# Performance work log

Hardware: AMD Instinct MI355X
Metric: run time of the kernel (lower is better)

## Reference

```python
import jax, jax.numpy as jnp
import numpy as np

B, T, N, D, H = 8, 24, 512, 128, 8
HD = D // H
HID = int(D * 2.0)
SCALES = (1.0, 0.01)


def _l2norm(a):
    # F.normalize(dim=-1), eps=1e-12
    n = jnp.sqrt(jnp.sum(a * a, axis=-1, keepdims=True))
    return a / jnp.maximum(n, 1e-12)


def _layernorm(a, g, b):
    mu = a.mean(-1, keepdims=True)
    var = ((a - mu) ** 2).mean(-1, keepdims=True)
    return (a - mu) / jnp.sqrt(var + 1e-5) * g + b


def _fast_attention_layer(z, qkv_w, out_w, out_b):
    # z: [B,T,N,D]; qkv_w: [D,3D]; out_w: [2D,D]; out_b: [D]
    b, t, n, d = z.shape
    q, k, v = jnp.split(z @ qkv_w, 3, axis=-1)          # each [B,T,N,D]
    q = q.reshape(b, t, n, H, HD)
    k = k.reshape(b, t, n, H, HD)
    v = v.reshape(b, t, n, H, HD)
    qn = _l2norm(q)
    kn = _l2norm(k)
    # spatial linear attention (tokens = nodes, axis 2)
    kvs = jnp.einsum('btnhm,btnhd->bthmd', kn, v)
    num = jnp.einsum('btnhm,bthmd->btnhd', qn, kvs) + n * v
    den = jnp.einsum('btnhm,bthm->btnh', qn, kn.sum(axis=2))[..., None] + n
    out_s = (num / den).reshape(b, t, n, d)
    # temporal linear attention (tokens = time steps, axis 1)
    kvt = jnp.einsum('btnhm,btnhd->bnhmd', kn, v)
    numt = jnp.einsum('btnhm,bnhmd->btnhd', qn, kvt) + t * v
    dent = jnp.einsum('btnhm,bnhm->btnh', qn, kn.sum(axis=1))[..., None] + t
    out_t = (numt / dent).reshape(b, t, n, d)
    return jnp.concatenate([out_s, out_t], axis=-1) @ out_w + out_b


def setup_inputs() -> dict:
    key = jax.random.key(0)
    ks = jax.random.split(key, 20)
    s = 0.02
    inp = {
        'x': jax.random.normal(ks[0], (B, T, N, D), jnp.float32),
        'graph': jax.random.uniform(ks[1], (T, N, N), jnp.float32) / N,
        'qkv_w0': jax.random.normal(ks[2], (D, 3 * D), jnp.float32) * s,
        'out_w0': jax.random.normal(ks[3], (2 * D, D), jnp.float32) * s,
        'out_b0': jnp.zeros((D,), jnp.float32),
        'pw_w0': jax.random.normal(ks[4], (D, D), jnp.float32) * s,
        'pw_b0': jax.random.normal(ks[5], (D,), jnp.float32) * s,
        'qkv_w1': jax.random.normal(ks[6], (D, 3 * D), jnp.float32) * s,
        'out_w1': jax.random.normal(ks[7], (2 * D, D), jnp.float32) * s,
        'out_b1': jnp.zeros((D,), jnp.float32),
        'pw_w1': jax.random.normal(ks[8], (D, D), jnp.float32) * s,
        'pw_b1': jax.random.normal(ks[9], (D,), jnp.float32) * s,
        'fc1_w': jax.random.normal(ks[10], (D, HID), jnp.float32) * s,
        'fc1_b': jnp.zeros((HID,), jnp.float32),
        'fc2_w': jax.random.normal(ks[11], (HID, D), jnp.float32) * s,
        'fc2_b': jnp.zeros((D,), jnp.float32),
        'ln1_g': jnp.ones((D,), jnp.float32),
        'ln1_b': jnp.zeros((D,), jnp.float32),
        'ln2_g': jnp.ones((D,), jnp.float32),
        'ln2_b': jnp.zeros((D,), jnp.float32),
    }
    return inp


def reference(x, graph, qkv_w0, out_w0, out_b0, pw_w0, pw_b0,
              qkv_w1, out_w1, out_b1, pw_w1, pw_b1,
              fc1_w, fc1_b, fc2_w, fc2_b, ln1_g, ln1_b, ln2_g, ln2_b):
    # GraphPropagate (Ks=order=2): x_loc = [x, graph @ x]; dropout in eval mode
    x1 = jnp.einsum('tni,btid->btnd', graph, x)
    x_loc = (x, x1)
    layer_params = ((qkv_w0, out_w0, out_b0, pw_w0, pw_b0),
                    (qkv_w1, out_w1, out_b1, pw_w1, pw_b1))
    c = x
    x_glo = x
    for k in range(2):
        qkv_w, out_w, out_b, pw_w, pw_b = layer_params[k]
        att = _fast_attention_layer(x_loc[k], qkv_w, out_w, out_b)
        pw = c @ pw_w + pw_b
        x_glo = x_glo + att * pw * SCALES[k]
        c = att
    h = _layernorm(x + x_glo, ln1_g, ln1_b)
    mlp = jax.nn.relu(h @ fc1_w + fc1_b) @ fc2_w + fc2_b
    return _layernorm(h + mlp, ln2_g, ln2_b)
```

## Files before the change

### kernel.cpp

```cpp
#include <hip/hip_runtime.h>
#include <cstddef>

#define Bb 8
#define Tt 24
#define Nn 512
#define Dd 128
#define Hh 8

typedef unsigned short u16;
using short8 = __attribute__((ext_vector_type(8))) short;
using f32x4  = __attribute__((ext_vector_type(4))) float;

__device__ __forceinline__ float b2f(u16 u) {
  union { unsigned u; float f; } w; w.u = ((unsigned)u) << 16; return w.f;
}
__device__ __forceinline__ u16 f2b(float f) {
  union { float f; unsigned u; } w; w.f = f;
  unsigned r = w.u + 0x7FFFu + ((w.u >> 16) & 1u);
  return (u16)(r >> 16);
}

__device__ __forceinline__ void mm_phase(const u16* __restrict__ A,
                                         const u16* __restrict__ BT,
                                         int K, int m0,
                                         u16* sA, u16* sB, f32x4 acc[4][4])
{
  const int tid = threadIdx.x;
  const int l = tid & 63, wid = tid >> 6;
  const int wm = (wid >> 1) << 6, wn = (wid & 1) << 6;
  int a_off[4], b_off[4];
#pragma unroll
  for (int i = 0; i < 4; ++i) {
    int ra = wm + i * 16 + (l & 15);
    a_off[i] = ((ra << 6) + ((l >> 4) << 4)) ^ ((ra & 7) << 4);
    int rb = wn + i * 16 + (l & 15);
    b_off[i] = ((rb << 6) + ((l >> 4) << 4)) ^ ((rb & 7) << 4);
  }
  const int r0 = tid >> 2, s0 = tid & 3;
  const int r1 = r0 + 64;
  const int w0 = ((r0 << 6) + (s0 << 4)) ^ ((r0 & 7) << 4);
  const int w1 = ((r1 << 6) + (s0 << 4)) ^ ((r1 & 7) << 4);
  const size_t aR0 = (size_t)(m0 + r0) * K, aR1 = (size_t)(m0 + r1) * K;
  const size_t bR0 = (size_t)r0 * K, bR1 = (size_t)r1 * K;
  const int ks = s0 * 8;
  for (int k0 = 0; k0 < K; k0 += 32) {
    short8 a0 = *(const short8*)(A + aR0 + k0 + ks);
    short8 a1 = *(const short8*)(A + aR1 + k0 + ks);
    short8 b0 = *(const short8*)(BT + bR0 + k0 + ks);
    short8 b1 = *(const short8*)(BT + bR1 + k0 + ks);
    __syncthreads();
    *(short8*)((char*)sA + w0) = a0;
    *(short8*)((char*)sA + w1) = a1;
    *(short8*)((char*)sB + w0) = b0;
    *(short8*)((char*)sB + w1) = b1;
    __syncthreads();
    short8 af[4], bf_[4];
#pragma unroll
    for (int i = 0; i < 4; ++i) {
      af[i]  = *(const short8*)((const char*)sA + a_off[i]);
      bf_[i] = *(const short8*)((const char*)sB + b_off[i]);
    }
#pragma unroll
    for (int mi = 0; mi < 4; ++mi)
#pragma unroll
      for (int ni = 0; ni < 4; ++ni)
        acc[mi][ni] = __builtin_amdgcn_mfma_f32_16x16x32_bf16(
            af[mi], bf_[ni], acc[mi][ni], 0, 0, 0);
  }
}

template <int OUTBF16, int RELU>
__device__ __forceinline__ void gemm_mfma_body(
    const u16* __restrict__ A, const u16* __restrict__ BT,
    const float* __restrict__ bias, void* __restrict__ Cv,
    int N, int K, int m0, int n0)
{
  __shared__ u16 sA[4096];
  __shared__ u16 sB[4096];
  f32x4 acc[4][4] = {};
  mm_phase(A, BT + (size_t)n0 * K, K, m0, sA, sB, acc);
  const int l = threadIdx.x & 63, wid = threadIdx.x >> 6;
  const int wm = (wid >> 1) << 6, wn = (wid & 1) << 6;
  const int cr = (l >> 4) << 2, cc = l & 15;
#pragma unroll
  for (int mi = 0; mi < 4; ++mi) {
    int rowb = m0 + wm + mi * 16 + cr;
#pragma unroll
    for (int ni = 0; ni < 4; ++ni) {
      int col = n0 + wn + ni * 16 + cc;
      float bb = bias ? bias[col] : 0.f;
#pragma unroll
      for (int r = 0; r < 4; ++r) {
        float v = acc[mi][ni][r] + bb;
        if (RELU) v = fmaxf(v, 0.f);
        size_t idx = (size_t)(rowb + r) * N + col;
        if (OUTBF16) ((u16*)Cv)[idx] = f2b(v);
        else         ((float*)Cv)[idx] = v;
      }
    }
  }
}

template <int OUTBF16, int RELU>
__global__ __launch_bounds__(256) void gemm_mfma_k(
    const u16* __restrict__ A, const u16* __restrict__ BT,
    const float* __restrict__ bias, void* __restrict__ C, int N, int K)
{
  gemm_mfma_body<OUTBF16, RELU>(A, BT, bias, C, N, K,
                                blockIdx.y * 128, blockIdx.x * 128);
}

__global__ __launch_bounds__(256) void gemm_mfma_graph(
    const u16* __restrict__ g, const u16* __restrict__ xT, u16* __restrict__ x1)
{
  const int bt = blockIdx.z, t = bt % Tt;
  gemm_mfma_body<1, 0>(g + (size_t)t * Nn * Nn, xT + (size_t)bt * Dd * Nn,
                       nullptr, x1 + (size_t)bt * Nn * Dd,
                       Dd, Nn, blockIdx.y * 128, 0);
}

__global__ __launch_bounds__(256) void gemm_og0(
    const u16* __restrict__ cat, const u16* __restrict__ outT, const float* __restrict__ ob,
    const u16* __restrict__ xb,  const u16* __restrict__ pwT,  const float* __restrict__ pb,
    u16* __restrict__ gp0, u16* __restrict__ att0)
{
  __shared__ u16 sA[4096], sB[4096];
  const int m0 = blockIdx.x * 128;
  f32x4 accP[4][4] = {};
  mm_phase(xb, pwT, 128, m0, sA, sB, accP);
  f32x4 accO[4][4] = {};
  mm_phase(cat, outT, 256, m0, sA, sB, accO);
  const int l = threadIdx.x & 63, wid = threadIdx.x >> 6;
  const int wm = (wid >> 1) << 6, wn = (wid & 1) << 6;
  const int cr = (l >> 4) << 2, cc = l & 15;
#pragma unroll
  for (int mi = 0; mi < 4; ++mi) {
    int rowb = m0 + wm + mi * 16 + cr;
#pragma unroll
    for (int ni = 0; ni < 4; ++ni) {
      int col = wn + ni * 16 + cc;
      float obv = ob[col], pbv = pb[col];
#pragma unroll
      for (int r = 0; r < 4; ++r) {
        size_t idx = (size_t)(rowb + r) * 128 + col;
        float attv = accO[mi][ni][r] + obv;
        float pwv  = accP[mi][ni][r] + pbv;
        att0[idx] = f2b(attv);
        gp0[idx] = f2b(attv * pwv);
      }
    }
  }
}

__global__ __launch_bounds__(256) void gemm_og1(
    const u16* __restrict__ cat, const u16* __restrict__ outT, const float* __restrict__ ob,
    const u16* __restrict__ att0, const u16* __restrict__ pwT, const float* __restrict__ pb,
    const u16* __restrict__ gp0, const float* __restrict__ x,
    const float* __restrict__ g, const float* __restrict__ be,
    u16* __restrict__ h16)
{
  __shared__ __align__(16) u16 smem[128 * 136];
  __shared__ float sg[128], sbt[128];
  u16* sA = smem;
  u16* sB = smem + 4096;
  if (threadIdx.x < 128) { sg[threadIdx.x] = g[threadIdx.x]; sbt[threadIdx.x] = be[threadIdx.x]; }
  const int m0 = blockIdx.x * 128;
  f32x4 accP[4][4] = {};
  mm_phase(att0, pwT, 128, m0, sA, sB, accP);
  f32x4 accO[4][4] = {};
  mm_phase(cat, outT, 256, m0, sA, sB, accO);
  const int l = threadIdx.x & 63, wid = threadIdx.x >> 6;
  const int wm = (wid >> 1) << 6, wn = (wid & 1) << 6;
  const int cr = (l >> 4) << 2, cc = l & 15;
  __syncthreads();
#pragma unroll
  for (int mi = 0; mi < 4; ++mi) {
    int lrow = wm + mi * 16 + cr;
#pragma unroll
    for (int ni = 0; ni < 4; ++ni) {
      int col = wn + ni * 16 + cc;
      float obv = ob[col], pbv = pb[col];
#pragma unroll
      for (int r = 0; r < 4; ++r) {
        size_t idx = (size_t)(m0 + lrow + r) * 128 + col;
        float attv = accO[mi][ni][r] + obv;
        float pwv  = accP[mi][ni][r] + pbv;
        float hpre = 2.f * x[idx] + b2f(gp0[idx]) + attv * pwv * 0.01f;
        smem[(lrow + r) * 136 + col] = f2b(hpre);
      }
    }
  }
  __syncthreads();
  const int row = threadIdx.x >> 1, half = threadIdx.x & 1;
  const u16* rp = smem + row * 136 + half * 64;
  float s = 0.f, ss = 0.f;
#pragma unroll
  for (int j8 = 0; j8 < 8; ++j8) {
    short8 v = *(const short8*)(rp + j8 * 8);
#pragma unroll
    for (int j = 0; j < 8; ++j) { float f = b2f((u16)v[j]); s += f; ss += f * f; }
  }
  s += __shfl_xor(s, 1);
  ss += __shfl_xor(ss, 1);
  float mu = s * (1.f / 128.f);
  float rstd = rsqrtf(ss * (1.f / 128.f) - mu * mu + 1e-5f);
  size_t gbase = (size_t)(m0 + row) * 128 + half * 64;
#pragma unroll
  for (int j8 = 0; j8 < 8; ++j8) {
    short8 v = *(const short8*)(rp + j8 * 8);
    short8 o;
#pragma unroll
    for (int j = 0; j < 8; ++j) {
      int col = half * 64 + j8 * 8 + j;
      o[j] = (short)f2b((b2f((u16)v[j]) - mu) * rstd * sg[col] + sbt[col]);
    }
    *(short8*)(h16 + gbase + j8 * 8) = o;
  }
}

__global__ __launch_bounds__(256) void gemm_fc2ln(
    const u16* __restrict__ hid, const u16* __restrict__ fc2T, const float* __restrict__ fb,
    const u16* __restrict__ h16, const float* __restrict__ g, const float* __restrict__ be,
    float* __restrict__ out)
{
  __shared__ __align__(16) u16 smem[128 * 136];
  __shared__ float sg[128], sbt[128];
  u16* sA = smem;
  u16* sB = smem + 4096;
  if (threadIdx.x < 128) { sg[threadIdx.x] = g[threadIdx.x]; sbt[threadIdx.x] = be[threadIdx.x]; }
  const int m0 = blockIdx.x * 128;
  f32x4 accO[4][4] = {};
  mm_phase(hid, fc2T, 256, m0, sA, sB, accO);
  const int l = threadIdx.x & 63, wid = threadIdx.x >> 6;
  const int wm = (wid >> 1) << 6, wn = (wid & 1) << 6;
  const int cr = (l >> 4) << 2, cc = l & 15;
  __syncthreads();
#pragma unroll
  for (int mi = 0; mi < 4; ++mi) {
    int lrow = wm + mi * 16 + cr;
#pragma unroll
    for (int ni = 0; ni < 4; ++ni) {
      int col = wn + ni * 16 + cc;
      float fbv = fb[col];
#pragma unroll
      for (int r = 0; r < 4; ++r) {
        size_t idx = (size_t)(m0 + lrow + r) * 128 + col;
        float hpre = b2f(h16[idx]) + accO[mi][ni][r] + fbv;
        smem[(lrow + r) * 136 + col] = f2b(hpre);
      }
    }
  }
  __syncthreads();
  const int row = threadIdx.x >> 1, half = threadIdx.x & 1;
  const u16* rp = smem + row * 136 + half * 64;
  float s = 0.f, ss = 0.f;
#pragma unroll
  for (int j8 = 0; j8 < 8; ++j8) {
    short8 v = *(const short8*)(rp + j8 * 8);
#pragma unroll
    for (int j = 0; j < 8; ++j) { float f = b2f((u16)v[j]); s += f; ss += f * f; }
  }
  s += __shfl_xor(s, 1);
  ss += __shfl_xor(ss, 1);
  float mu = s * (1.f / 128.f);
  float rstd = rsqrtf(ss * (1.f / 128.f) - mu * mu + 1e-5f);
  size_t gbase = (size_t)(m0 + row) * 128 + half * 64;
#pragma unroll
  for (int j8 = 0; j8 < 8; ++j8) {
    short8 v = *(const short8*)(rp + j8 * 8);
    float4 o0, o1;
#pragma unroll
    for (int j = 0; j < 8; ++j) {
      int col = half * 64 + j8 * 8 + j;
      float y = (b2f((u16)v[j]) - mu) * rstd * sg[col] + sbt[col];
      if (j < 4) ((float*)&o0)[j] = y; else ((float*)&o1)[j - 4] = y;
    }
    *(float4*)(out + gbase + j8 * 8) = o0;
    *(float4*)(out + gbase + j8 * 8 + 4) = o1;
  }
}

__global__ __launch_bounds__(256) void qknorm(const u16* __restrict__ qkv,
                                              float* __restrict__ inv, size_t nidx)
{
  size_t idx = (size_t)blockIdx.x * 256 + threadIdx.x;
  if (idx >= nidx) return;
  size_t row = idx >> 4;
  int g = (int)(idx & 15);
  const u16* p = qkv + row * 384 + g * 16;
  short8 a = *(const short8*)p;
  short8 b = *(const short8*)(p + 8);
  float ss = 0.f;
#pragma unroll
  for (int j = 0; j < 8; ++j) {
    float f0 = b2f((u16)a[j]), f1 = b2f((u16)b[j]);
    ss += f0 * f0 + f1 * f1;
  }
  inv[idx] = 1.f / fmaxf(sqrtf(ss), 1e-12f);
}

__global__ __launch_bounds__(256) void cvt_f32_bf16(const float* __restrict__ src,
                                                    u16* __restrict__ dst, size_t n8)
{
  size_t i = (size_t)blockIdx.x * 256 + threadIdx.x;
  if (i >= n8) return;
  const float4* s = (const float4*)src;
  float4 u = s[i * 2], v = s[i * 2 + 1];
  short8 o;
  o[0] = (short)f2b(u.x); o[1] = (short)f2b(u.y);
  o[2] = (short)f2b(u.z); o[3] = (short)f2b(u.w);
  o[4] = (short)f2b(v.x); o[5] = (short)f2b(v.y);
  o[6] = (short)f2b(v.z); o[7] = (short)f2b(v.w);
  *(short8*)(dst + i * 8) = o;
}

__global__ __launch_bounds__(256) void transpose_cvt(const float* __restrict__ src,
                                                     u16* __restrict__ dst,
                                                     int R, int C)
{
  __shared__ u16 tile[64][65];
  const int tid = threadIdx.x;
  src += (size_t)blockIdx.z * R * C;
  dst += (size_t)blockIdx.z * R * C;
  const int c0 = blockIdx.x * 64, r0 = blockIdx.y * 64;
  const int tx = tid & 63, ty = tid >> 6;
#pragma unroll
  for (int i = 0; i < 64; i += 4)
    tile[ty + i][tx] = f2b(src[(size_t)(r0 + ty + i) * C + c0 + tx]);
  __syncthreads();
#pragma unroll
  for (int i = 0; i < 64; i += 4)
    dst[(size_t)(c0 + ty + i) * R + r0 + tx] = tile[tx][ty + i];
}

__global__ __launch_bounds__(256) void cvt_transpose_x(const float* __restrict__ src,
                                                       u16* __restrict__ xb,
                                                       u16* __restrict__ xT)
{
  __shared__ u16 tile[64][65];
  const int tid = threadIdx.x;
  const size_t zo = (size_t)blockIdx.z * Nn * Dd;
  src += zo; xb += zo; xT += zo;
  const int c0 = blockIdx.x * 64, r0 = blockIdx.y * 64;
  const int tx = tid & 63, ty = tid >> 6;
#pragma unroll
  for (int i = 0; i < 64; i += 4) {
    u16 b = f2b(src[(size_t)(r0 + ty + i) * Dd + c0 + tx]);
    tile[ty + i][tx] = b;
    xb[(size_t)(r0 + ty + i) * Dd + c0 + tx] = b;
  }
  __syncthreads();
#pragma unroll
  for (int i = 0; i < 64; i += 4)
    xT[(size_t)(c0 + ty + i) * Nn + r0 + tx] = tile[tx][ty + i];
}

__global__ __launch_bounds__(256) void spatial_stats(const u16* __restrict__ qkv,
                                                     const float* __restrict__ qkn,
                                                     float* __restrict__ kvs2,
                                                     float* __restrict__ ksum)
{
  __shared__ u16 sKT[16 * 512];
  __shared__ u16 sVT[16 * 512];
  __shared__ float red[4][16][16];
  __shared__ float red2[4][16];
  const int bt = blockIdx.x, h = blockIdx.y;
  const int tid = threadIdx.x;

  u16 kr[2][16], vr[2][16];
#pragma unroll
  for (int r = 0; r < 2; ++r) {
    int n = tid * 2 + r;
    size_t rowg = (size_t)bt * 512 + n;
    size_t base = rowg * 384;
    float inv = qkn[rowg * 16 + 8 + h];
    short8 k0 = *(const short8*)(qkv + base + 128 + h * 16);
    short8 k1 = *(const short8*)(qkv + base + 136 + h * 16);
    short8 v0 = *(const short8*)(qkv + base + 256 + h * 16);
    short8 v1 = *(const short8*)(qkv + base + 264 + h * 16);
#pragma unroll
    for (int j = 0; j < 8; ++j) {
      kr[r][j]     = f2b(b2f((u16)k0[j]) * inv);
      kr[r][j + 8] = f2b(b2f((u16)k1[j]) * inv);
      vr[r][j] = (u16)v0[j]; vr[r][j + 8] = (u16)v1[j];
    }
  }
#pragma unroll
  for (int m = 0; m < 16; ++m) {
    unsigned pk = (unsigned)kr[0][m] | ((unsigned)kr[1][m] << 16);
    unsigned pv = (unsigned)vr[0][m] | ((unsigned)vr[1][m] << 16);
    int wa = ((m << 10) + (tid << 2)) ^ ((m & 7) << 4);
    *(unsigned*)((char*)sKT + wa) = pk;
    *(unsigned*)((char*)sVT + wa) = pv;
  }
  __syncthreads();

  const int l = tid & 63, w = tid >> 6;
  const int fr = l & 15, tq = l >> 4;
  short8 ones;
#pragma unroll
  for (int j = 0; j < 8; ++j) ones[j] = (short)0x3F80;
  f32x4 acc = {}, acs = {};
#pragma unroll
  for (int kk = 0; kk < 4; ++kk) {
    int noff = w * 128 + kk * 32 + tq * 8;
    int ra = ((fr << 10) + (noff << 1)) ^ ((fr & 7) << 4);
    short8 afr = *(const short8*)((const char*)sKT + ra);
    short8 bfr = *(const short8*)((const char*)sVT + ra);
    acc = __builtin_amdgcn_mfma_f32_16x16x32_bf16(afr, bfr, acc, 0, 0, 0);
    acs = __builtin_amdgcn_mfma_f32_16x16x32_bf16(afr, ones, acs, 0, 0, 0);
  }
#pragma unroll
  for (int r = 0; r < 4; ++r) red[w][tq * 4 + r][fr] = acc[r];
  if (fr == 0) {
#pragma unroll
    for (int r = 0; r < 4; ++r) red2[w][tq * 4 + r] = acs[r];
  }
  __syncthreads();
  const size_t o = (size_t)bt * 8 + h;
  {
    int m = tid >> 4, d = tid & 15;
    float s = red[0][m][d] + red[1][m][d] + red[2][m][d] + red[3][m][d];
    kvs2[o * 256 + d * 16 + m] = s;
  }
  if (tid < 16) {
    float s = red2[0][tid] + red2[1][tid] + red2[2][tid] + red2[3][tid];
    ksum[o * 16 + tid] = s;
  }
}

__global__ __launch_bounds__(256) void temporal_stats(const u16* __restrict__ qkv,
                                                      const float* __restrict__ qkn,
                                                      float* __restrict__ kvt,
                                                      float* __restrict__ kst)
{
  __shared__ u16 sKT[128 * 32];
  __shared__ u16 sVT[128 * 32];
  const int nn = blockIdx.x, b = blockIdx.y;
  const int tid = threadIdx.x;
  if (tid < 128) {
    short8 z = {};
    int wa = ((tid << 6) + 48) ^ ((tid & 3) << 4);
    *(short8*)((char*)sKT + wa) = z;
    *(short8*)((char*)sVT + wa) = z;
  }
  for (int idx = tid; idx < 384; idx += 256) {
    int t = idx >> 4, c8 = idx & 15;
    size_t rowg = ((size_t)(b * 24 + t) * 512) + nn;
    float inv = qkn[rowg * 16 + 8 + (c8 >> 1)];
    short8 kv = *(const short8*)(qkv + rowg * 384 + 128 + c8 * 8);
    short8 vv = *(const short8*)(qkv + rowg * 384 + 256 + c8 * 8);
#pragma unroll
    for (int j = 0; j < 8; ++j) {
      int c = c8 * 8 + j;
      int wa = ((c << 6) + (t << 1)) ^ ((c & 3) << 4);
      *(u16*)((char*)sKT + wa) = f2b(b2f((u16)kv[j]) * inv);
      *(u16*)((char*)sVT + wa) = (u16)vv[j];
    }
  }
  __syncthreads();
  const int l = tid & 63, w = tid >> 6;
  const int fr = l & 15, tq = l >> 4;
  const size_t nb = (size_t)b * 512 + nn;
  short8 ones;
#pragma unroll
  for (int j = 0; j < 8; ++j) ones[j] = (short)0x3F80;
#pragma unroll
  for (int hi = 0; hi < 2; ++hi) {
    int h = w * 2 + hi;
    int c = h * 16 + fr;
    int ra = ((c << 6) + (tq << 4)) ^ ((c & 3) << 4);
    short8 afr = *(const short8*)((const char*)sKT + ra);
    short8 bfr = *(const short8*)((const char*)sVT + ra);
    f32x4 z = {};
    f32x4 acc = __builtin_amdgcn_mfma_f32_16x16x32_bf16(afr, bfr, z, 0, 0, 0);
    f32x4 acs = __builtin_amdgcn_mfma_f32_16x16x32_bf16(afr, ones, z, 0, 0, 0);
#pragma unroll
    for (int r = 0; r < 4; ++r)
      kvt[nb * 2048 + (size_t)(tq * 4 + r) * 128 + h * 16 + fr] = acc[r];
    if (fr == 0) {
#pragma unroll
      for (int r = 0; r < 4; ++r)
        kst[(nb * 8 + h) * 16 + tq * 4 + r] = acs[r];
    }
  }
}

__global__ __launch_bounds__(256) void attn_apply(const u16* __restrict__ qkv,
                                                  const float* __restrict__ qkn,
                                                  const float* __restrict__ kvs2,
                                                  const float* __restrict__ kss,
                                                  const float* __restrict__ kvt,
                                                  const float* __restrict__ kst,
                                                  u16* __restrict__ out_cat)
{
  __shared__ float s_kvt[2][2048];
  const int nn0 = blockIdx.x * 2, b = blockIdx.y;
  const int t0 = blockIdx.z * 8;
  const int tid = threadIdx.x;
  const int sub = tid >> 7, cl = tid & 127;
  const int nn = nn0 + sub;
  const size_t nb = (size_t)b * 512 + nn;
  for (int i = cl; i < 2048; i += 128) s_kvt[sub][i] = kvt[nb * 2048 + i];
  __syncthreads();
  const int hh = cl >> 4, d = cl & 15;
  const float kst_d = kst[(nb * 8 + hh) * 16 + d];
  for (int t = t0; t < t0 + 8; ++t) {
    const size_t row = ((size_t)(b * 24 + t) * 512) + nn;
    const u16* qp = qkv + row * 384 + hh * 16;
    short8 q0 = *(const short8*)qp;
    short8 q1 = *(const short8*)(qp + 8);
    const float inv = qkn[row * 16 + hh];
    float qf[16];
#pragma unroll
    for (int j = 0; j < 8; ++j) {
      qf[j] = b2f((u16)q0[j]);
      qf[j + 8] = b2f((u16)q1[j]);
    }
    const size_t sbase = ((size_t)(b * 24 + t) * 8 + hh) * 256 + d * 16;
    const float4* M4 = (const float4*)(kvs2 + sbase);
    float4 m0 = M4[0], m1 = M4[1], m2 = M4[2], m3 = M4[3];
    float accs = qf[0] * m0.x + qf[1] * m0.y + qf[2] * m0.z + qf[3] * m0.w;
    accs = fmaf(qf[4], m1.x, fmaf(qf[5], m1.y, fmaf(qf[6], m1.z, fmaf(qf[7], m1.w, accs))));
    accs = fmaf(qf[8], m2.x, fmaf(qf[9], m2.y, fmaf(qf[10], m2.z, fmaf(qf[11], m2.w, accs))));
    accs = fmaf(qf[12], m3.x, fmaf(qf[13], m3.y, fmaf(qf[14], m3.z, fmaf(qf[15], m3.w, accs))));
    float dps = qf[d] * kss[((size_t)(b * 24 + t) * 8 + hh) * 16 + d];
    dps += __shfl_xor(dps, 1);
    dps += __shfl_xor(dps, 2);
    dps += __shfl_xor(dps, 4);
    dps += __shfl_xor(dps, 8);
    float acct = 0.f;
#pragma unroll
    for (int mI = 0; mI < 16; ++mI)
      acct = fmaf(qf[mI], s_kvt[sub][mI * 128 + cl], acct);
    float dpt = qf[d] * kst_d;
    dpt += __shfl_xor(dpt, 1);
    dpt += __shfl_xor(dpt, 2);
    dpt += __shfl_xor(dpt, 4);
    dpt += __shfl_xor(dpt, 8);
    float vv = b2f(qkv[row * 384 + 256 + cl]);
    out_cat[row * 256 + cl]       = f2b((accs * inv + 512.f * vv) / (dps * inv + 512.f));
    out_cat[row * 256 + 128 + cl] = f2b((acct * inv + 24.f * vv) / (dpt * inv + 24.f));
  }
}

extern "C" void kernel_launch(void* const* d_in, const int* in_sizes, int n_in,
                              void* d_out, int out_size, void* d_ws, size_t ws_size,
                              hipStream_t stream)
{
  const float* x      = (const float*)d_in[0];
  const float* graph  = (const float*)d_in[1];
  const float* qkv_w0 = (const float*)d_in[2];
  const float* out_w0 = (const float*)d_in[3];
  const float* out_b0 = (const float*)d_in[4];
  const float* pw_w0  = (const float*)d_in[5];
  const float* pw_b0  = (const float*)d_in[6];
  const float* qkv_w1 = (const float*)d_in[7];
  const float* out_w1 = (const float*)d_in[8];
  const float* out_b1 = (const float*)d_in[9];
  const float* pw_w1  = (const float*)d_in[10];
  const float* pw_b1  = (const float*)d_in[11];
  const float* fc1_w  = (const float*)d_in[12];
  const float* fc1_b  = (const float*)d_in[13];
  const float* fc2_w  = (const float*)d_in[14];
  const float* fc2_b  = (const float*)d_in[15];
  const float* ln1_g  = (const float*)d_in[16];
  const float* ln1_b  = (const float*)d_in[17];
  const float* ln2_g  = (const float*)d_in[18];
  const float* ln2_b  = (const float*)d_in[19];
  float* out = (float*)d_out;

  auto al = [](size_t v) { return (v + 255) & ~(size_t)255; };
  const size_t Rb = 12288;
  const size_t fixed = al((size_t)Tt * Nn * Nn * 2) + 2 * al((size_t)384 * 128 * 2)
                     + 2 * al((size_t)128 * 256 * 2) + 2 * al((size_t)128 * 128 * 2)
                     + al((size_t)256 * 128 * 2) + al((size_t)128 * 256 * 2);
  const size_t perb = al(Rb * 768) + al(Rb * 512) + 4 * al(Rb * 256) + al(Rb * 512)
                    + al(Rb * 64)
                    + al((size_t)Tt * 8 * 256 * 4) + al((size_t)Tt * 8 * 16 * 4)
                    + al((size_t)Nn * 8 * 256 * 4) + al((size_t)Nn * 8 * 16 * 4);
  int CB = 8;
  while (CB > 1 && fixed + (size_t)CB * perb > ws_size) CB >>= 1;
  const size_t Mc = (size_t)CB * Rb;

  char* cur = (char*)d_ws;
  auto alloc = [&](size_t bytes) { char* p = cur; cur += (bytes + 255) & ~(size_t)255; return p; };
  u16* g_b16 = (u16*)alloc((size_t)Tt * Nn * Nn * 2);
  u16* qkvT0 = (u16*)alloc((size_t)384 * 128 * 2);
  u16* qkvT1 = (u16*)alloc((size_t)384 * 128 * 2);
  u16* outT0 = (u16*)alloc((size_t)128 * 256 * 2);
  u16* outT1 = (u16*)alloc((size_t)128 * 256 * 2);
  u16* pwT0  = (u16*)alloc((size_t)128 * 128 * 2);
  u16* pwT1  = (u16*)alloc((size_t)128 * 128 * 2);
  u16* fc1T  = (u16*)alloc((size_t)256 * 128 * 2);
  u16* fc2T  = (u16*)alloc((size_t)128 * 256 * 2);
  u16* qkvb  = (u16*)alloc(Mc * 768);
  u16* catb  = (u16*)alloc(Mc * 512);
  u16* x1b   = (u16*)alloc(Mc * 256);
  u16* att0  = (u16*)alloc(Mc * 256);
  u16* xb    = (u16*)alloc(Mc * 256);
  u16* xT    = (u16*)alloc(Mc * 256);
  u16* gp0   = (u16*)alloc(Mc * 512);
  float* qkn = (float*)alloc(Mc * 64);
  float* kvs = (float*)alloc((size_t)CB * Tt * 8 * 256 * 4);
  float* kss = (float*)alloc((size_t)CB * Tt * 8 * 16 * 4);
  float* kvt = (float*)alloc((size_t)CB * Nn * 8 * 256 * 4);
  float* kst = (float*)alloc((size_t)CB * Nn * 8 * 16 * 4);

  dim3 blk(256);
  cvt_f32_bf16<<<dim3((Tt * Nn * Nn / 8 + 255) / 256), blk, 0, stream>>>(
      graph, g_b16, (size_t)Tt * Nn * Nn / 8);
  transpose_cvt<<<dim3(6, 2, 1), blk, 0, stream>>>(qkv_w0, qkvT0, 128, 384);
  transpose_cvt<<<dim3(6, 2, 1), blk, 0, stream>>>(qkv_w1, qkvT1, 128, 384);
  transpose_cvt<<<dim3(2, 4, 1), blk, 0, stream>>>(out_w0, outT0, 256, 128);
  transpose_cvt<<<dim3(2, 4, 1), blk, 0, stream>>>(out_w1, outT1, 256, 128);
  transpose_cvt<<<dim3(2, 2, 1), blk, 0, stream>>>(pw_w0, pwT0, 128, 128);
  transpose_cvt<<<dim3(2, 2, 1), blk, 0, stream>>>(pw_w1, pwT1, 128, 128);
  transpose_cvt<<<dim3(4, 2, 1), blk, 0, stream>>>(fc1_w, fc1T, 128, 256);
  transpose_cvt<<<dim3(2, 4, 1), blk, 0, stream>>>(fc2_w, fc2T, 256, 128);

  const int MB = (int)(Mc / 128);
  const int nchunk = Bb / CB;
  for (int c = 0; c < nchunk; ++c) {
    const size_t off = (size_t)c * Mc * 128;
    const float* xc = x + off;
    float* outc = out + off;

    cvt_transpose_x<<<dim3(2, 8, CB * Tt), blk, 0, stream>>>(xc, xb, xT);
    gemm_mfma_graph<<<dim3(1, 4, CB * Tt), blk, 0, stream>>>(g_b16, xT, x1b);

    gemm_mfma_k<1, 0><<<dim3(3, MB), blk, 0, stream>>>(xb, qkvT0, nullptr, qkvb, 384, 128);
    qknorm<<<dim3((unsigned)(Mc / 16)), blk, 0, stream>>>(qkvb, qkn, Mc * 16);
    spatial_stats<<<dim3(CB * Tt, Hh), blk, 0, stream>>>(qkvb, qkn, kvs, kss);
    temporal_stats<<<dim3(Nn, CB), blk, 0, stream>>>(qkvb, qkn, kvt, kst);
    attn_apply<<<dim3(Nn / 2, CB, 3), blk, 0, stream>>>(qkvb, qkn, kvs, kss, kvt, kst, catb);
    gemm_og0<<<dim3(MB), blk, 0, stream>>>(catb, outT0, out_b0, xb, pwT0, pw_b0,
                                           gp0, att0);

    gemm_mfma_k<1, 0><<<dim3(3, MB), blk, 0, stream>>>(x1b, qkvT1, nullptr, qkvb, 384, 128);
    qknorm<<<dim3((unsigned)(Mc / 16)), blk, 0, stream>>>(qkvb, qkn, Mc * 16);
    spatial_stats<<<dim3(CB * Tt, Hh), blk, 0, stream>>>(qkvb, qkn, kvs, kss);
    temporal_stats<<<dim3(Nn, CB), blk, 0, stream>>>(qkvb, qkn, kvt, kst);
    attn_apply<<<dim3(Nn / 2, CB, 3), blk, 0, stream>>>(qkvb, qkn, kvs, kss, kvt, kst, catb);
    u16* h16 = qkvb;
    gemm_og1<<<dim3(MB), blk, 0, stream>>>(catb, outT1, out_b1, att0, pwT1, pw_b1,
                                           gp0, xc, ln1_g, ln1_b, h16);

    gemm_mfma_k<1, 1><<<dim3(2, MB), blk, 0, stream>>>(h16, fc1T, fc1_b, catb, 256, 128);
    gemm_fc2ln<<<dim3(MB), blk, 0, stream>>>(catb, fc2T, fc2_b, h16, ln2_g, ln2_b, outc);
  }

  (void)in_sizes; (void)n_in; (void)out_size;
}
```

Measured before the change: 658.0 us.

## Load GEMM tiles directly into LDS and streamline attention denominators

The GEMM main loop now uses global_load_lds to move A and B tiles straight from global memory into shared memory. This drops the register round trip and the XOR swizzle, so the LDS layout becomes plain row-major. In attn_apply, the spatial and temporal denominators are computed as full per-thread dot products from vectorized loads instead of butterfly shuffle reductions. Divisions are replaced with hardware reciprocals. Risks: the unswizzled LDS layout may cause bank conflicts on the fragment reads, the loads are no longer issued ahead of the barrier, and rcpf is less precise than a true divide.

```diff
diff --git a/kernel.cpp b/kernel.cpp
--- a/kernel.cpp
+++ b/kernel.cpp
@@ -20,6 +20,12 @@
   return (u16)(r >> 16);
 }
 
+__device__ __forceinline__ void gld16(const u16* g, u16* s) {
+  __builtin_amdgcn_global_load_lds(
+      (const __attribute__((address_space(1))) unsigned int*)g,
+      (__attribute__((address_space(3))) unsigned int*)s, 16, 0, 0);
+}
+
 __device__ __forceinline__ void mm_phase(const u16* __restrict__ A,
                                          const u16* __restrict__ BT,
                                          int K, int m0,
@@ -31,28 +37,23 @@
   int a_off[4], b_off[4];
 #pragma unroll
   for (int i = 0; i < 4; ++i) {
-    int ra = wm + i * 16 + (l & 15);
-    a_off[i] = ((ra << 6) + ((l >> 4) << 4)) ^ ((ra & 7) << 4);
-    int rb = wn + i * 16 + (l & 15);
-    b_off[i] = ((rb << 6) + ((l >> 4) << 4)) ^ ((rb & 7) << 4);
-  }
-  const int r0 = tid >> 2, s0 = tid & 3;
-  const int r1 = r0 + 64;
-  const int w0 = ((r0 << 6) + (s0 << 4)) ^ ((r0 & 7) << 4);
-  const int w1 = ((r1 << 6) + (s0 << 4)) ^ ((r1 & 7) << 4);
-  const size_t aR0 = (size_t)(m0 + r0) * K, aR1 = (size_t)(m0 + r1) * K;
-  const size_t bR0 = (size_t)r0 * K, bR1 = (size_t)r1 * K;
-  const int ks = s0 * 8;
+    a_off[i] = (wm + i * 16 + (l & 15)) * 64 + (l >> 4) * 16;
+    b_off[i] = (wn + i * 16 + (l & 15)) * 64 + (l >> 4) * 16;
+  }
+  const int gr = l >> 2, kqo = (l & 3) * 8;
+  const int R0 = wid * 32 + gr, R1 = wid * 32 + 16 + gr;
+  u16* dA0 = sA + (wid * 2 + 0) * 512;
+  u16* dA1 = sA + (wid * 2 + 1) * 512;
+  u16* dB0 = sB + (wid * 2 + 0) * 512;
+  u16* dB1 = sB + (wid * 2 + 1) * 512;
+  const size_t aR0 = (size_t)(m0 + R0) * K, aR1 = (size_t)(m0 + R1) * K;
+  const size_t bR0 = (size_t)R0 * K, bR1 = (size_t)R1 * K;
   for (int k0 = 0; k0 < K; k0 += 32) {
-    short8 a0 = *(const short8*)(A + aR0 + k0 + ks);
-    short8 a1 = *(const short8*)(A + aR1 + k0 + ks);
-    short8 b0 = *(const short8*)(BT + bR0 + k0 + ks);
-    short8 b1 = *(const short8*)(BT + bR1 + k0 + ks);
     __syncthreads();
-    *(short8*)((char*)sA + w0) = a0;
-    *(short8*)((char*)sA + w1) = a1;
-    *(short8*)((char*)sB + w0) = b0;
-    *(short8*)((char*)sB + w1) = b1;
+    gld16(A + aR0 + k0 + kqo, dA0);
+    gld16(A + aR1 + k0 + kqo, dA1);
+    gld16(BT + bR0 + k0 + kqo, dB0);
+    gld16(BT + bR1 + k0 + kqo, dB1);
     __syncthreads();
     short8 af[4], bf_[4];
 #pragma unroll
@@ -504,7 +505,15 @@
   for (int i = cl; i < 2048; i += 128) s_kvt[sub][i] = kvt[nb * 2048 + i];
   __syncthreads();
   const int hh = cl >> 4, d = cl & 15;
-  const float kst_d = kst[(nb * 8 + hh) * 16 + d];
+  float kstr[16];
+  {
+    const float4* k4 = (const float4*)(kst + (nb * 8 + hh) * 16);
+#pragma unroll
+    for (int i = 0; i < 4; ++i) {
+      float4 v = k4[i];
+      kstr[i * 4] = v.x; kstr[i * 4 + 1] = v.y; kstr[i * 4 + 2] = v.z; kstr[i * 4 + 3] = v.w;
+    }
+  }
   for (int t = t0; t < t0 + 8; ++t) {
     const size_t row = ((size_t)(b * 24 + t) * 512) + nn;
     const u16* qp = qkv + row * 384 + hh * 16;
@@ -517,30 +526,34 @@
       qf[j] = b2f((u16)q0[j]);
       qf[j + 8] = b2f((u16)q1[j]);
     }
-    const size_t sbase = ((size_t)(b * 24 + t) * 8 + hh) * 256 + d * 16;
-    const float4* M4 = (const float4*)(kvs2 + sbase);
-    float4 m0 = M4[0], m1 = M4[1], m2 = M4[2], m3 = M4[3];
-    float accs = qf[0] * m0.x + qf[1] * m0.y + qf[2] * m0.z + qf[3] * m0.w;
-    accs = fmaf(qf[4], m1.x, fmaf(qf[5], m1.y, fmaf(qf[6], m1.z, fmaf(qf[7], m1.w, accs))));
-    accs = fmaf(qf[8], m2.x, fmaf(qf[9], m2.y, fmaf(qf[10], m2.z, fmaf(qf[11], m2.w, accs))));
-    accs = fmaf(qf[12], m3.x, fmaf(qf[13], m3.y, fmaf(qf[14], m3.z, fmaf(qf[15], m3.w, accs))));
-    float dps = qf[d] * kss[((size_t)(b * 24 + t) * 8 + hh) * 16 + d];
-    dps += __shfl_xor(dps, 1);
-    dps += __shfl_xor(dps, 2);
-    dps += __shfl_xor(dps, 4);
-    dps += __shfl_xor(dps, 8);
-    float acct = 0.f;
-#pragma unroll
-    for (int mI = 0; mI < 16; ++mI)
+    const size_t hb = (size_t)(b * 24 + t) * 8 + hh;
+    const float4* M4 = (const float4*)(kvs2 + hb * 256 + d * 16);
+    float accs = 0.f;
+#pragma unroll
+    for (int i = 0; i < 4; ++i) {
+      float4 m = M4[i];
+      accs = fmaf(qf[i * 4], m.x, fmaf(qf[i * 4 + 1], m.y,
+             fmaf(qf[i * 4 + 2], m.z, fmaf(qf[i * 4 + 3], m.w, accs))));
+    }
+    const float4* K4 = (const float4*)(kss + hb * 16);
+    float dps = 0.f;
+#pragma unroll
+    for (int i = 0; i < 4; ++i) {
+      float4 m = K4[i];
+      dps = fmaf(qf[i * 4], m.x, fmaf(qf[i * 4 + 1], m.y,
+            fmaf(qf[i * 4 + 2], m.z, fmaf(qf[i * 4 + 3], m.w, dps))));
+    }
+    float acct = 0.f, dpt = 0.f;
+#pragma unroll
+    for (int mI = 0; mI < 16; ++mI) {
       acct = fmaf(qf[mI], s_kvt[sub][mI * 128 + cl], acct);
-    float dpt = qf[d] * kst_d;
-    dpt += __shfl_xor(dpt, 1);
-    dpt += __shfl_xor(dpt, 2);
-    dpt += __shfl_xor(dpt, 4);
-    dpt += __shfl_xor(dpt, 8);
+      dpt  = fmaf(qf[mI], kstr[mI], dpt);
+    }
     float vv = b2f(qkv[row * 384 + 256 + cl]);
-    out_cat[row * 256 + cl]       = f2b((accs * inv + 512.f * vv) / (dps * inv + 512.f));
-    out_cat[row * 256 + 128 + cl] = f2b((acct * inv + 24.f * vv) / (dpt * inv + 24.f));
+    float rs = __builtin_amdgcn_rcpf(fmaf(dps, inv, 512.f));
+    float rt = __builtin_amdgcn_rcpf(fmaf(dpt, inv, 24.f));
+    out_cat[row * 256 + cl]       = f2b(fmaf(accs, inv, 512.f * vv) * rs);
+    out_cat[row * 256 + 128 + cl] = f2b(fmaf(acct, inv, 24.f * vv) * rt);
   }
 }
 
```

Result: slower. 678.8 us (+3.2%).
